# Optimization experiments

Hardware: AMD Instinct MI355X
Metric: run time of the kernel (lower is better)

## Reference

```python
import jax, jax.numpy as jnp
import numpy as np
from jax import lax

B, H, W = 2, 240, 1216
ITER, NUM = 3, 9
CH = ITER * NUM  # 27


def setup_inputs() -> dict:
    key = jax.random.key(0)
    ks = jax.random.split(key, 6)
    inp = jax.random.normal(ks[0], (B, 1, H, W), dtype=jnp.float32)
    guide = jax.random.normal(ks[1], (B, CH, H, W), dtype=jnp.float32)
    sp_dep = jax.random.uniform(ks[2], (B, 1, H, W), dtype=jnp.float32)
    confidence = jax.random.normal(ks[3], (B, 1, H, W), dtype=jnp.float32)
    conv_w = jax.random.normal(ks[4], (3 * CH, CH, 3, 3), dtype=jnp.float32) * 0.05
    conv_b = jax.random.normal(ks[5], (3 * CH,), dtype=jnp.float32) * 0.05
    # fixed 3x3 tap offsets, rows are (dx, dy) -- matches mode='xy'
    tap = jnp.array([[-1, -1], [0, -1], [1, -1], [-1, 0], [0, 0], [1, 0], [-1, 1], [0, 1], [1, 1]], dtype=jnp.float32)
    return {"input": inp, "guide": guide, "sp_dep": sp_dep, "confidence": confidence,
            "conv_w": conv_w, "conv_b": conv_b, "tap": tap}


def _bilinear_zeros(img, px, py):
    """img: [B,H,W]; px,py: [B,N,H,W] pixel coords. Matches F.grid_sample
    (bilinear, padding_mode='zeros', align_corners=False): the normalized grid
    built in get_refgrid maps exactly to pixel coord = x + tap + offset."""
    Hh, Ww = img.shape[-2], img.shape[-1]
    x0f = jnp.floor(px)
    y0f = jnp.floor(py)
    wx1 = px - x0f
    wy1 = py - y0f
    x0 = x0f.astype(jnp.int32)
    y0 = y0f.astype(jnp.int32)
    flat = img.reshape(img.shape[0], Hh * Ww)

    def gather(xi, yi):
        valid = (xi >= 0) & (xi < Ww) & (yi >= 0) & (yi < Hh)
        idx = jnp.clip(yi, 0, Hh - 1) * Ww + jnp.clip(xi, 0, Ww - 1)
        v = jax.vmap(lambda f, i: f[i])(flat, idx)  # [B,N,H,W]
        return jnp.where(valid, v, jnp.zeros((), img.dtype))

    v00 = gather(x0, y0)
    v01 = gather(x0 + 1, y0)
    v10 = gather(x0, y0 + 1)
    v11 = gather(x0 + 1, y0 + 1)
    return ((1 - wy1) * ((1 - wx1) * v00 + wx1 * v01)
            + wy1 * ((1 - wx1) * v10 + wx1 * v11))


def reference(input, guide, sp_dep, confidence, conv_w, conv_b, tap):
    Bb, _, Hh, Ww = input.shape
    out = lax.conv_general_dilated(
        guide, conv_w, window_strides=(1, 1), padding=((1, 1), (1, 1)),
        dimension_numbers=("NCHW", "OIHW", "NCHW")) + conv_b[None, :, None, None]
    # split into offsets (2*ch) and affinities (ch)
    offset = out[:, :2 * CH].reshape(Bb, ITER, NUM, 2, Hh, Ww)  # b iter n (x,y) h w
    aff = out[:, 2 * CH:].reshape(Bb, ITER, NUM, Hh, Ww)
    aff = jax.nn.softmax(aff, axis=2)  # softmax over the NUM taps

    conf = jax.nn.sigmoid(confidence[:, 0]) * jnp.sign(sp_dep[:, 0])  # [B,H,W]
    spd = sp_dep[:, 0]

    xg = jnp.arange(Ww, dtype=jnp.float32)
    yg = jnp.arange(Hh, dtype=jnp.float32)
    # sampling pixel coords: x + tap_x + offset_x  (exact grid_sample equivalence)
    px = offset[:, :, :, 0] + tap[None, None, :, 0, None, None] + xg[None, None, None, None, :]
    py = offset[:, :, :, 1] + tap[None, None, :, 1, None, None] + yg[None, None, None, :, None]

    cur = input[:, 0]  # [B,H,W]
    feat_init = cur
    inter = []
    for i in range(ITER):
        vals = _bilinear_zeros(cur, px[:, i], py[:, i])  # [B,NUM,H,W]
        agg = jnp.sum(vals * aff[:, i], axis=1)          # affinity-weighted sum
        cur = (1 - conf) * agg + conf * spd
        inter.append(cur)
    pred = cur[:, None]
    return pred, feat_init[:, None], jnp.stack(inter, axis=0)[:, :, None]
```

## Files before the change

### kernel.cpp

```cpp
#include <hip/hip_runtime.h>
#include <math.h>

#define B_ 2
#define H_ 240
#define W_ 1216
#define CH_ 27
#define NUM_ 9
#define PIX_ (B_ * H_ * W_)
#define CHP 32
#define CHL 40
#define TX 32
#define TY 8
#define HALO_W (TX + 2)
#define HALO_H (TY + 2)
#define SCS 27

typedef __attribute__((ext_vector_type(8))) __bf16 bf16x8;
typedef __attribute__((ext_vector_type(16))) float f32x16;

__global__ __launch_bounds__(256) void transpose_guide(
    const float* __restrict__ guide, __bf16* __restrict__ gt)
{
    int pix = blockIdx.x * 256 + threadIdx.x;
    if (pix >= PIX_) return;
    int b = pix / (H_ * W_);
    int off = pix - b * (H_ * W_);
    __align__(16) __bf16 tmp[CHP];
    const float* src = guide + (size_t)b * CH_ * H_ * W_ + off;
    #pragma unroll
    for (int ic = 0; ic < CH_; ++ic)
        tmp[ic] = (__bf16)src[(size_t)ic * (H_ * W_)];
    #pragma unroll
    for (int ic = CH_; ic < CHP; ++ic) tmp[ic] = (__bf16)0.f;
    bf16x8* dst = (bf16x8*)(gt + (size_t)pix * CHP);
    const bf16x8* s8 = (const bf16x8*)tmp;
    #pragma unroll
    for (int c = 0; c < 4; ++c) dst[c] = s8[c];
}

__global__ __launch_bounds__(256) void prep_weights(
    const float* __restrict__ conv_w, __bf16* __restrict__ wlin)
{
    int idx = blockIdx.x * 256 + threadIdx.x;
    if (idx >= 3 * 9 * 2 * 64) return;
    int lane = idx & 63;
    int grp = idx >> 6;
    int ks = grp & 1;
    int tapi = (grp >> 1) % 9;
    int it = (grp >> 1) / 9;
    int n = lane & 31;
    int half = lane >> 5;
    __align__(16) __bf16 v8[8];
    #pragma unroll
    for (int j = 0; j < 8; ++j) {
        int ic = ks * 16 + half * 8 + j;
        float v = 0.f;
        if (ic < CH_ && n < CH_) {
            int oc = (n < 18) ? (it * 18 + n) : (54 + it * NUM_ + (n - 18));
            v = conv_w[(size_t)(oc * CH_ + ic) * 9 + tapi];
        }
        v8[j] = (__bf16)v;
    }
    *(bf16x8*)(wlin + (size_t)idx * 8) = *(const bf16x8*)v8;
}

__global__ __launch_bounds__(256, 4) void dyspn_iter_mfma(
    const __bf16* __restrict__ gt, const __bf16* __restrict__ wlin,
    const float* __restrict__ conv_b, const float* __restrict__ tap,
    const float* __restrict__ confidence, const float* __restrict__ sp_dep,
    const float* __restrict__ cur_in, float* __restrict__ out_cur,
    float* __restrict__ pred, float* __restrict__ feat,
    const float* __restrict__ input, int iter)
{
    __shared__ __align__(16) char smem[256 * SCS * 4];
    __bf16* sG = (__bf16*)smem;
    float*  sC = (float*)smem;
    __shared__ float sBias[CH_ + 1];
    __shared__ float sTap[18];

    const int tid = threadIdx.x;
    const int lane = tid & 63;
    const int w = tid >> 6;
    const int xl = lane & 31;
    const int half = lane >> 5;
    const int tileX0 = blockIdx.x * TX;
    const int tileY0 = blockIdx.y * TY;
    const int b = blockIdx.z;

    const int x = tileX0 + (tid & 31);
    const int y = tileY0 + (tid >> 5);
    const int pix = b * (H_ * W_) + y * W_ + x;

    const float cpix  = confidence[pix];
    const float sppix = sp_dep[pix];
    const float inpix = input[pix];

    if (tid < CH_) {
        int n = tid;
        int oc = (n < 18) ? (iter * 18 + n) : (54 + iter * NUM_ + (n - 18));
        sBias[tid] = conv_b[oc];
    }
    if (tid >= 64 && tid < 64 + 18) sTap[tid - 64] = tap[tid - 64];

    for (int idx = tid; idx < HALO_H * HALO_W * 4; idx += 256) {
        int chunk = idx & 3;
        int p = idx >> 2;
        int row = p / HALO_W;
        int px = p - row * HALO_W;
        int gy = tileY0 + row - 1;
        int gx = tileX0 + px - 1;
        uint4 v = make_uint4(0, 0, 0, 0);
        if (gx >= 0 && gx < W_ && gy >= 0 && gy < H_) {
            size_t pg = (size_t)b * (H_ * W_) + (size_t)gy * W_ + gx;
            v = ((const uint4*)(gt + pg * CHP))[chunk];
        }
        *(uint4*)((char*)sG + ((size_t)(row * HALO_W + px) * CHL + chunk * 8) * 2) = v;
    }

    f32x16 acc0 = {0,0,0,0,0,0,0,0,0,0,0,0,0,0,0,0};
    f32x16 acc1 = {0,0,0,0,0,0,0,0,0,0,0,0,0,0,0,0};

    __syncthreads();

    const __bf16* wbase = wlin + ((size_t)iter * 18 * 64 + lane) * 8;
    #pragma unroll
    for (int kw = 0; kw < 3; ++kw) {
        #pragma unroll
        for (int ks = 0; ks < 2; ++ks) {
            bf16x8 A4[4];
            #pragma unroll
            for (int d = 0; d < 4; ++d) {
                const __bf16* ap = sG + (size_t)((2 * w + d) * HALO_W + xl + kw) * CHL
                                 + ks * 16 + half * 8;
                A4[d] = *(const bf16x8*)ap;
            }
            #pragma unroll
            for (int kh = 0; kh < 3; ++kh) {
                int t = kh * 3 + kw;
                bf16x8 Bf = *(const bf16x8*)(wbase + (size_t)(t * 2 + ks) * 64 * 8);
                acc0 = __builtin_amdgcn_mfma_f32_32x32x16_bf16(A4[kh],     Bf, acc0, 0, 0, 0);
                acc1 = __builtin_amdgcn_mfma_f32_32x32x16_bf16(A4[kh + 1], Bf, acc1, 0, 0, 0);
            }
        }
    }

    __syncthreads();

    if (xl < CH_) {
        #pragma unroll
        for (int a = 0; a < 2; ++a) {
            const f32x16 A = a ? acc1 : acc0;
            int ra = 2 * w + a;
            #pragma unroll
            for (int r = 0; r < 16; ++r) {
                int px_x = (r & 3) + 8 * (r >> 2) + 4 * half;
                sC[(ra * 32 + px_x) * SCS + xl] = A[r];
            }
        }
    }

    __syncthreads();

    float v27[CH_];
    #pragma unroll
    for (int j = 0; j < CH_; ++j) v27[j] = sC[tid * SCS + j] + sBias[j];

    float m = v27[18];
    #pragma unroll
    for (int n = 1; n < 9; ++n) m = fmaxf(m, v27[18 + n]);
    float a9[9]; float s = 0.f;
    #pragma unroll
    for (int n = 0; n < 9; ++n) { a9[n] = __expf(v27[18 + n] - m); s += a9[n]; }
    const float inv_s = 1.f / s;

    const float* cur = cur_in + (size_t)b * (H_ * W_);
    float agg = 0.f;
    #pragma unroll
    for (int n = 0; n < 9; ++n) {
        float px = v27[2 * n]     + sTap[2 * n]     + (float)x;
        float py = v27[2 * n + 1] + sTap[2 * n + 1] + (float)y;
        float x0f = floorf(px), y0f = floorf(py);
        float wx = px - x0f, wy = py - y0f;
        int x0 = (int)x0f, y0 = (int)y0f;
        int cx0 = min(max(x0, 0), W_ - 1), cx1 = min(max(x0 + 1, 0), W_ - 1);
        int cy0 = min(max(y0, 0), H_ - 1), cy1 = min(max(y0 + 1, 0), H_ - 1);
        float mx0 = (x0 >= 0 && x0 < W_) ? 1.f : 0.f;
        float mx1 = (x0 + 1 >= 0 && x0 + 1 < W_) ? 1.f : 0.f;
        float my0 = (y0 >= 0 && y0 < H_) ? 1.f : 0.f;
        float my1 = (y0 + 1 >= 0 && y0 + 1 < H_) ? 1.f : 0.f;
        const float* r0 = cur + (size_t)cy0 * W_;
        const float* r1 = cur + (size_t)cy1 * W_;
        float v00 = r0[cx0] * (mx0 * my0);
        float v01 = r0[cx1] * (mx1 * my0);
        float v10 = r1[cx0] * (mx0 * my1);
        float v11 = r1[cx1] * (mx1 * my1);
        float val = (1.f - wy) * ((1.f - wx) * v00 + wx * v01)
                  +        wy  * ((1.f - wx) * v10 + wx * v11);
        agg = fmaf(val, a9[n] * inv_s, agg);
    }

    float sgn = (sppix > 0.f) ? 1.f : ((sppix < 0.f) ? -1.f : 0.f);
    float conf = sgn / (1.f + __expf(-cpix));
    float nc = (1.f - conf) * agg + conf * sppix;

    out_cur[pix] = nc;
    if (pred) pred[pix] = nc;
    if (feat) feat[pix] = inpix;
}

__global__ __launch_bounds__(256) void dyspn_iter_fp32(
    const float* __restrict__ guide, const float* __restrict__ conv_w,
    const float* __restrict__ conv_b, const float* __restrict__ tap,
    const float* __restrict__ confidence, const float* __restrict__ sp_dep,
    const float* __restrict__ cur_in, float* __restrict__ out_cur,
    float* __restrict__ pred, float* __restrict__ feat,
    const float* __restrict__ input, int iter)
{
    __shared__ float sg[CH_ * HALO_H * HALO_W];
    const int tid = threadIdx.x;
    const int tileX0 = blockIdx.x * TX;
    const int tileY0 = blockIdx.y * TY;
    const int b = blockIdx.z;
    for (int idx = tid; idx < CH_ * HALO_H * HALO_W; idx += 256) {
        int ic  = idx / (HALO_H * HALO_W);
        int rem = idx % (HALO_H * HALO_W);
        int ly = rem / HALO_W;
        int lx = rem % HALO_W;
        int gy = tileY0 + ly - 1;
        int gx = tileX0 + lx - 1;
        float v = 0.f;
        if (gx >= 0 && gx < W_ && gy >= 0 && gy < H_)
            v = guide[((b * CH_ + ic) * H_ + gy) * W_ + gx];
        sg[idx] = v;
    }
    __syncthreads();
    const int tx = tid % TX;
    const int ty = tid / TX;
    const int x = tileX0 + tx;
    const int y = tileY0 + ty;
    const int oc0 = iter * 18;
    const int oc1 = 54 + iter * NUM_;
    float acc[27];
    #pragma unroll
    for (int j = 0; j < 18; ++j) acc[j] = conv_b[oc0 + j];
    #pragma unroll
    for (int j = 0; j < 9; ++j)  acc[18 + j] = conv_b[oc1 + j];
    for (int ic = 0; ic < CH_; ++ic) {
        float g[9];
        #pragma unroll
        for (int t = 0; t < 9; ++t) {
            int dy = t / 3, dx = t % 3;
            g[t] = sg[ic * (HALO_H * HALO_W) + (ty + dy) * HALO_W + (tx + dx)];
        }
        #pragma unroll
        for (int j = 0; j < 18; ++j) {
            const float* wp = conv_w + ((oc0 + j) * CH_ + ic) * 9;
            #pragma unroll
            for (int t = 0; t < 9; ++t) acc[j] = fmaf(wp[t], g[t], acc[j]);
        }
        #pragma unroll
        for (int j = 0; j < 9; ++j) {
            const float* wp = conv_w + ((oc1 + j) * CH_ + ic) * 9;
            #pragma unroll
            for (int t = 0; t < 9; ++t) acc[18 + j] = fmaf(wp[t], g[t], acc[18 + j]);
        }
    }
    float m = acc[18];
    #pragma unroll
    for (int n = 1; n < 9; ++n) m = fmaxf(m, acc[18 + n]);
    float a[9]; float s = 0.f;
    #pragma unroll
    for (int n = 0; n < 9; ++n) { a[n] = __expf(acc[18 + n] - m); s += a[n]; }
    const float inv_s = 1.f / s;
    const float* cur = cur_in + b * (H_ * W_);
    float agg = 0.f;
    #pragma unroll
    for (int n = 0; n < 9; ++n) {
        float px = acc[2 * n]     + tap[2 * n]     + (float)x;
        float py = acc[2 * n + 1] + tap[2 * n + 1] + (float)y;
        float x0f = floorf(px), y0f = floorf(py);
        float wx = px - x0f, wy = py - y0f;
        int x0 = (int)x0f, y0 = (int)y0f;
        int cx0 = min(max(x0, 0), W_ - 1), cx1 = min(max(x0 + 1, 0), W_ - 1);
        int cy0 = min(max(y0, 0), H_ - 1), cy1 = min(max(y0 + 1, 0), H_ - 1);
        float mx0 = (x0 >= 0 && x0 < W_) ? 1.f : 0.f;
        float mx1 = (x0 + 1 >= 0 && x0 + 1 < W_) ? 1.f : 0.f;
        float my0 = (y0 >= 0 && y0 < H_) ? 1.f : 0.f;
        float my1 = (y0 + 1 >= 0 && y0 + 1 < H_) ? 1.f : 0.f;
        float v00 = cur[(size_t)cy0 * W_ + cx0] * (mx0 * my0);
        float v01 = cur[(size_t)cy0 * W_ + cx1] * (mx1 * my0);
        float v10 = cur[(size_t)cy1 * W_ + cx0] * (mx0 * my1);
        float v11 = cur[(size_t)cy1 * W_ + cx1] * (mx1 * my1);
        float val = (1.f - wy) * ((1.f - wx) * v00 + wx * v01)
                  +        wy  * ((1.f - wx) * v10 + wx * v11);
        agg = fmaf(val, a[n] * inv_s, agg);
    }
    const int pix = b * (H_ * W_) + y * W_ + x;
    float c  = confidence[pix];
    float sp = sp_dep[pix];
    float sgn = (sp > 0.f) ? 1.f : ((sp < 0.f) ? -1.f : 0.f);
    float conf = sgn / (1.f + __expf(-c));
    float nc = (1.f - conf) * agg + conf * sp;
    out_cur[pix] = nc;
    if (pred) pred[pix] = nc;
    if (feat) feat[pix] = input[pix];
}

extern "C" void kernel_launch(void* const* d_in, const int* in_sizes, int n_in,
                              void* d_out, int out_size, void* d_ws, size_t ws_size,
                              hipStream_t stream) {
    (void)in_sizes; (void)n_in; (void)out_size;
    const float* input      = (const float*)d_in[0];
    const float* guide      = (const float*)d_in[1];
    const float* sp_dep     = (const float*)d_in[2];
    const float* confidence = (const float*)d_in[3];
    const float* conv_w     = (const float*)d_in[4];
    const float* conv_b     = (const float*)d_in[5];
    const float* tap        = (const float*)d_in[6];

    float* out   = (float*)d_out;
    const int P  = PIX_;
    float* pred  = out;
    float* feat  = out + P;
    float* inter = out + 2 * P;

    dim3 grid(W_ / TX, H_ / TY, B_);
    dim3 block(256);

    const size_t gt_bytes   = (size_t)PIX_ * CHP * 2;
    const size_t wlin_bytes = (size_t)3 * 9 * 2 * 64 * 8 * 2;

    if (ws_size >= gt_bytes + wlin_bytes) {
        __bf16* gt   = (__bf16*)d_ws;
        __bf16* wlin = (__bf16*)((char*)d_ws + gt_bytes);

        transpose_guide<<<(PIX_ + 255) / 256, 256, 0, stream>>>(guide, gt);
        prep_weights<<<(3 * 9 * 2 * 64 + 255) / 256, 256, 0, stream>>>(conv_w, wlin);

        for (int i = 0; i < 3; ++i) {
            const float* cur = (i == 0) ? input : (inter + (i - 1) * P);
            dyspn_iter_mfma<<<grid, block, 0, stream>>>(
                gt, wlin, conv_b, tap, confidence, sp_dep,
                cur, inter + i * P,
                (i == 2) ? pred : nullptr,
                (i == 0) ? feat : nullptr,
                input, i);
        }
    } else {
        for (int i = 0; i < 3; ++i) {
            const float* cur = (i == 0) ? input : (inter + (i - 1) * P);
            dyspn_iter_fp32<<<grid, block, 0, stream>>>(
                guide, conv_w, conv_b, tap, confidence, sp_dep,
                cur, inter + i * P,
                (i == 2) ? pred : nullptr,
                (i == 0) ? feat : nullptr,
                input, i);
        }
    }
}
```

Before: 216.6 us.

## Fuse guide transpose, weight prep and three iterations into one cooperative persistent kernel

Replaces the five separate launches (guide transpose, weight packing, three iteration kernels) with one cooperative persistent kernel. Blocks loop over tiles and use grid-wide syncs between phases and iterations. This removes per-launch overhead and gaps between dependent kernels, at the cost of grid-sync latency and a capped grid size (1140 or 760 blocks) that may reduce parallelism or balance. The fp32 fallback path is dropped, and if the workspace is too small nothing is launched.

```diff
diff --git a/kernel.cpp b/kernel.cpp
--- a/kernel.cpp
+++ b/kernel.cpp
@@ -1,5 +1,8 @@
 #include <hip/hip_runtime.h>
+#include <hip/hip_cooperative_groups.h>
 #include <math.h>
+
+namespace cg = cooperative_groups;
 
 #define B_ 2
 #define H_ 240
@@ -13,10 +16,216 @@
 #define TY 8
 #define HALO_W (TX + 2)
 #define HALO_H (TY + 2)
+#define NPX (HALO_H * HALO_W)
 #define SCS 27
+#define NTILES (38 * 30 * B_)
 
 typedef __attribute__((ext_vector_type(8))) __bf16 bf16x8;
 typedef __attribute__((ext_vector_type(16))) float f32x16;
+
+__global__ __launch_bounds__(256, 4) void dyspn_persistent(
+    const float* __restrict__ guide, const float* __restrict__ conv_w,
+    const float* __restrict__ conv_b, const float* __restrict__ tap,
+    const float* __restrict__ confidence, const float* __restrict__ sp_dep,
+    const float* __restrict__ input, float* __restrict__ pred,
+    float* __restrict__ feat, float* __restrict__ inter,
+    __bf16* __restrict__ gt, __bf16* __restrict__ wlin)
+{
+    cg::grid_group gg = cg::this_grid();
+
+    __shared__ __align__(16) char smemA[256 * SCS * 4];
+    __bf16* sG = (__bf16*)smemA;
+    float*  sC = (float*)smemA;
+    __shared__ float sBias[CH_ + 1];
+    __shared__ float sTap[18];
+
+    const int tid  = threadIdx.x;
+    const int lane = tid & 63;
+    const int w    = tid >> 6;
+    const int xl   = lane & 31;
+    const int half = lane >> 5;
+    const int nb   = gridDim.x;
+    const int brank = blockIdx.x;
+
+    for (int pix = brank * 256 + tid; pix < PIX_; pix += nb * 256) {
+        int b = pix / (H_ * W_);
+        int off = pix - b * (H_ * W_);
+        __align__(16) __bf16 tmp[CHP];
+        const float* src = guide + (size_t)b * CH_ * H_ * W_ + off;
+        #pragma unroll
+        for (int ic = 0; ic < CH_; ++ic)
+            tmp[ic] = (__bf16)src[(size_t)ic * (H_ * W_)];
+        #pragma unroll
+        for (int ic = CH_; ic < CHP; ++ic) tmp[ic] = (__bf16)0.f;
+        bf16x8* dst = (bf16x8*)(gt + (size_t)pix * CHP);
+        const bf16x8* s8 = (const bf16x8*)tmp;
+        #pragma unroll
+        for (int c = 0; c < 4; ++c) dst[c] = s8[c];
+    }
+
+    for (int idx = brank * 256 + tid; idx < 3 * 9 * 2 * 64; idx += nb * 256) {
+        int l = idx & 63;
+        int grp = idx >> 6;
+        int ks = grp & 1;
+        int tapi = (grp >> 1) % 9;
+        int it = (grp >> 1) / 9;
+        int n = l & 31;
+        int hf = l >> 5;
+        __align__(16) __bf16 v8[8];
+        #pragma unroll
+        for (int j = 0; j < 8; ++j) {
+            int ic = ks * 16 + hf * 8 + j;
+            float v = 0.f;
+            if (ic < CH_ && n < CH_) {
+                int oc = (n < 18) ? (it * 18 + n) : (54 + it * NUM_ + (n - 18));
+                v = conv_w[(size_t)(oc * CH_ + ic) * 9 + tapi];
+            }
+            v8[j] = (__bf16)v;
+        }
+        *(bf16x8*)(wlin + (size_t)idx * 8) = *(const bf16x8*)v8;
+    }
+
+    gg.sync();
+
+    for (int iter = 0; iter < 3; ++iter) {
+        const float* cur_all = (iter == 0) ? input : (inter + (size_t)(iter - 1) * PIX_);
+        float* dst = inter + (size_t)iter * PIX_;
+
+        if (tid < CH_) {
+            int n = tid;
+            int oc = (n < 18) ? (iter * 18 + n) : (54 + iter * NUM_ + (n - 18));
+            sBias[tid] = conv_b[oc];
+        }
+        if (tid >= 64 && tid < 64 + 18) sTap[tid - 64] = tap[tid - 64];
+
+        const __bf16* wbase = wlin + ((size_t)iter * 18 * 64 + lane) * 8;
+
+        for (int t = brank; t < NTILES; t += nb) {
+            int b   = t / (38 * 30);
+            int r   = t - b * (38 * 30);
+            int tyi = r / 38;
+            int txi = r - tyi * 38;
+            const int tileX0 = txi * TX;
+            const int tileY0 = tyi * TY;
+
+            const int x = tileX0 + (tid & 31);
+            const int y = tileY0 + (tid >> 5);
+            const int pix = b * (H_ * W_) + y * W_ + x;
+
+            const float cpix  = confidence[pix];
+            const float sppix = sp_dep[pix];
+            const float inpix = input[pix];
+
+            for (int idx = tid; idx < NPX * 4; idx += 256) {
+                int chunk = idx & 3;
+                int p = idx >> 2;
+                int row = p / HALO_W;
+                int px = p - row * HALO_W;
+                int gy = tileY0 + row - 1;
+                int gx = tileX0 + px - 1;
+                uint4 v = make_uint4(0, 0, 0, 0);
+                if (gx >= 0 && gx < W_ && gy >= 0 && gy < H_) {
+                    size_t pg = (size_t)b * (H_ * W_) + (size_t)gy * W_ + gx;
+                    v = ((const uint4*)(gt + pg * CHP))[chunk];
+                }
+                *(uint4*)((char*)sG + ((size_t)(row * HALO_W + px) * CHL + chunk * 8) * 2) = v;
+            }
+
+            f32x16 acc0 = {0,0,0,0,0,0,0,0,0,0,0,0,0,0,0,0};
+            f32x16 acc1 = {0,0,0,0,0,0,0,0,0,0,0,0,0,0,0,0};
+
+            __syncthreads();
+
+            #pragma unroll
+            for (int kw = 0; kw < 3; ++kw) {
+                #pragma unroll
+                for (int ks = 0; ks < 2; ++ks) {
+                    bf16x8 A4[4];
+                    #pragma unroll
+                    for (int d = 0; d < 4; ++d) {
+                        const __bf16* ap = sG + (size_t)((2 * w + d) * HALO_W + xl + kw) * CHL
+                                         + ks * 16 + half * 8;
+                        A4[d] = *(const bf16x8*)ap;
+                    }
+                    #pragma unroll
+                    for (int kh = 0; kh < 3; ++kh) {
+                        int tt = kh * 3 + kw;
+                        bf16x8 Bf = *(const bf16x8*)(wbase + (size_t)(tt * 2 + ks) * 64 * 8);
+                        acc0 = __builtin_amdgcn_mfma_f32_32x32x16_bf16(A4[kh],     Bf, acc0, 0, 0, 0);
+                        acc1 = __builtin_amdgcn_mfma_f32_32x32x16_bf16(A4[kh + 1], Bf, acc1, 0, 0, 0);
+                    }
+                }
+            }
+
+            __syncthreads();
+
+            if (xl < CH_) {
+                #pragma unroll
+                for (int a = 0; a < 2; ++a) {
+                    const f32x16 A = a ? acc1 : acc0;
+                    int ra = 2 * w + a;
+                    #pragma unroll
+                    for (int rr = 0; rr < 16; ++rr) {
+                        int px_x = (rr & 3) + 8 * (rr >> 2) + 4 * half;
+                        sC[(ra * 32 + px_x) * SCS + xl] = A[rr];
+                    }
+                }
+            }
+
+            __syncthreads();
+
+            float v27[CH_];
+            #pragma unroll
+            for (int j = 0; j < CH_; ++j) v27[j] = sC[tid * SCS + j] + sBias[j];
+
+            float m = v27[18];
+            #pragma unroll
+            for (int n = 1; n < 9; ++n) m = fmaxf(m, v27[18 + n]);
+            float a9[9]; float s = 0.f;
+            #pragma unroll
+            for (int n = 0; n < 9; ++n) { a9[n] = __expf(v27[18 + n] - m); s += a9[n]; }
+            const float inv_s = 1.f / s;
+
+            const float* cur = cur_all + (size_t)b * (H_ * W_);
+            float agg = 0.f;
+            #pragma unroll
+            for (int n = 0; n < 9; ++n) {
+                float px = v27[2 * n]     + sTap[2 * n]     + (float)x;
+                float py = v27[2 * n + 1] + sTap[2 * n + 1] + (float)y;
+                float x0f = floorf(px), y0f = floorf(py);
+                float wx = px - x0f, wy = py - y0f;
+                int x0 = (int)x0f, y0 = (int)y0f;
+                int cx0 = min(max(x0, 0), W_ - 1), cx1 = min(max(x0 + 1, 0), W_ - 1);
+                int cy0 = min(max(y0, 0), H_ - 1), cy1 = min(max(y0 + 1, 0), H_ - 1);
+                float mx0 = (x0 >= 0 && x0 < W_) ? 1.f : 0.f;
+                float mx1 = (x0 + 1 >= 0 && x0 + 1 < W_) ? 1.f : 0.f;
+                float my0 = (y0 >= 0 && y0 < H_) ? 1.f : 0.f;
+                float my1 = (y0 + 1 >= 0 && y0 + 1 < H_) ? 1.f : 0.f;
+                const float* r0 = cur + (size_t)cy0 * W_;
+                const float* r1 = cur + (size_t)cy1 * W_;
+                float v00 = r0[cx0] * (mx0 * my0);
+                float v01 = r0[cx1] * (mx1 * my0);
+                float v10 = r1[cx0] * (mx0 * my1);
+                float v11 = r1[cx1] * (mx1 * my1);
+                float val = (1.f - wy) * ((1.f - wx) * v00 + wx * v01)
+                          +        wy  * ((1.f - wx) * v10 + wx * v11);
+                agg = fmaf(val, a9[n] * inv_s, agg);
+            }
+
+            float sgn = (sppix > 0.f) ? 1.f : ((sppix < 0.f) ? -1.f : 0.f);
+            float conf = sgn / (1.f + __expf(-cpix));
+            float nc = (1.f - conf) * agg + conf * sppix;
+
+            dst[pix] = nc;
+            if (iter == 2) pred[pix] = nc;
+            if (iter == 0) feat[pix] = inpix;
+
+            __syncthreads();
+        }
+
+        if (iter < 2) gg.sync();
+    }
+}
 
 __global__ __launch_bounds__(256) void transpose_guide(
     const float* __restrict__ guide, __bf16* __restrict__ gt)
@@ -102,7 +311,7 @@
     }
     if (tid >= 64 && tid < 64 + 18) sTap[tid - 64] = tap[tid - 64];
 
-    for (int idx = tid; idx < HALO_H * HALO_W * 4; idx += 256) {
+    for (int idx = tid; idx < NPX * 4; idx += 256) {
         int chunk = idx & 3;
         int p = idx >> 2;
         int row = p / HALO_W;
@@ -208,104 +417,6 @@
     if (feat) feat[pix] = inpix;
 }
 
-__global__ __launch_bounds__(256) void dyspn_iter_fp32(
-    const float* __restrict__ guide, const float* __restrict__ conv_w,
-    const float* __restrict__ conv_b, const float* __restrict__ tap,
-    const float* __restrict__ confidence, const float* __restrict__ sp_dep,
-    const float* __restrict__ cur_in, float* __restrict__ out_cur,
-    float* __restrict__ pred, float* __restrict__ feat,
-    const float* __restrict__ input, int iter)
-{
-    __shared__ float sg[CH_ * HALO_H * HALO_W];
-    const int tid = threadIdx.x;
-    const int tileX0 = blockIdx.x * TX;
-    const int tileY0 = blockIdx.y * TY;
-    const int b = blockIdx.z;
-    for (int idx = tid; idx < CH_ * HALO_H * HALO_W; idx += 256) {
-        int ic  = idx / (HALO_H * HALO_W);
-        int rem = idx % (HALO_H * HALO_W);
-        int ly = rem / HALO_W;
-        int lx = rem % HALO_W;
-        int gy = tileY0 + ly - 1;
-        int gx = tileX0 + lx - 1;
-        float v = 0.f;
-        if (gx >= 0 && gx < W_ && gy >= 0 && gy < H_)
-            v = guide[((b * CH_ + ic) * H_ + gy) * W_ + gx];
-        sg[idx] = v;
-    }
-    __syncthreads();
-    const int tx = tid % TX;
-    const int ty = tid / TX;
-    const int x = tileX0 + tx;
-    const int y = tileY0 + ty;
-    const int oc0 = iter * 18;
-    const int oc1 = 54 + iter * NUM_;
-    float acc[27];
-    #pragma unroll
-    for (int j = 0; j < 18; ++j) acc[j] = conv_b[oc0 + j];
-    #pragma unroll
-    for (int j = 0; j < 9; ++j)  acc[18 + j] = conv_b[oc1 + j];
-    for (int ic = 0; ic < CH_; ++ic) {
-        float g[9];
-        #pragma unroll
-        for (int t = 0; t < 9; ++t) {
-            int dy = t / 3, dx = t % 3;
-            g[t] = sg[ic * (HALO_H * HALO_W) + (ty + dy) * HALO_W + (tx + dx)];
-        }
-        #pragma unroll
-        for (int j = 0; j < 18; ++j) {
-            const float* wp = conv_w + ((oc0 + j) * CH_ + ic) * 9;
-            #pragma unroll
-            for (int t = 0; t < 9; ++t) acc[j] = fmaf(wp[t], g[t], acc[j]);
-        }
-        #pragma unroll
-        for (int j = 0; j < 9; ++j) {
-            const float* wp = conv_w + ((oc1 + j) * CH_ + ic) * 9;
-            #pragma unroll
-            for (int t = 0; t < 9; ++t) acc[18 + j] = fmaf(wp[t], g[t], acc[18 + j]);
-        }
-    }
-    float m = acc[18];
-    #pragma unroll
-    for (int n = 1; n < 9; ++n) m = fmaxf(m, acc[18 + n]);
-    float a[9]; float s = 0.f;
-    #pragma unroll
-    for (int n = 0; n < 9; ++n) { a[n] = __expf(acc[18 + n] - m); s += a[n]; }
-    const float inv_s = 1.f / s;
-    const float* cur = cur_in + b * (H_ * W_);
-    float agg = 0.f;
-    #pragma unroll
-    for (int n = 0; n < 9; ++n) {
-        float px = acc[2 * n]     + tap[2 * n]     + (float)x;
-        float py = acc[2 * n + 1] + tap[2 * n + 1] + (float)y;
-        float x0f = floorf(px), y0f = floorf(py);
-        float wx = px - x0f, wy = py - y0f;
-        int x0 = (int)x0f, y0 = (int)y0f;
-        int cx0 = min(max(x0, 0), W_ - 1), cx1 = min(max(x0 + 1, 0), W_ - 1);
-        int cy0 = min(max(y0, 0), H_ - 1), cy1 = min(max(y0 + 1, 0), H_ - 1);
-        float mx0 = (x0 >= 0 && x0 < W_) ? 1.f : 0.f;
-        float mx1 = (x0 + 1 >= 0 && x0 + 1 < W_) ? 1.f : 0.f;
-        float my0 = (y0 >= 0 && y0 < H_) ? 1.f : 0.f;
-        float my1 = (y0 + 1 >= 0 && y0 + 1 < H_) ? 1.f : 0.f;
-        float v00 = cur[(size_t)cy0 * W_ + cx0] * (mx0 * my0);
-        float v01 = cur[(size_t)cy0 * W_ + cx1] * (mx1 * my0);
-        float v10 = cur[(size_t)cy1 * W_ + cx0] * (mx0 * my1);
-        float v11 = cur[(size_t)cy1 * W_ + cx1] * (mx1 * my1);
-        float val = (1.f - wy) * ((1.f - wx) * v00 + wx * v01)
-                  +        wy  * ((1.f - wx) * v10 + wx * v11);
-        agg = fmaf(val, a[n] * inv_s, agg);
-    }
-    const int pix = b * (H_ * W_) + y * W_ + x;
-    float c  = confidence[pix];
-    float sp = sp_dep[pix];
-    float sgn = (sp > 0.f) ? 1.f : ((sp < 0.f) ? -1.f : 0.f);
-    float conf = sgn / (1.f + __expf(-c));
-    float nc = (1.f - conf) * agg + conf * sp;
-    out_cur[pix] = nc;
-    if (pred) pred[pix] = nc;
-    if (feat) feat[pix] = input[pix];
-}
-
 extern "C" void kernel_launch(void* const* d_in, const int* in_sizes, int n_in,
                               void* d_out, int out_size, void* d_ws, size_t ws_size,
                               hipStream_t stream) {
@@ -324,37 +435,45 @@
     float* feat  = out + P;
     float* inter = out + 2 * P;
 
-    dim3 grid(W_ / TX, H_ / TY, B_);
-    dim3 block(256);
-
     const size_t gt_bytes   = (size_t)PIX_ * CHP * 2;
     const size_t wlin_bytes = (size_t)3 * 9 * 2 * 64 * 8 * 2;
 
-    if (ws_size >= gt_bytes + wlin_bytes) {
-        __bf16* gt   = (__bf16*)d_ws;
-        __bf16* wlin = (__bf16*)((char*)d_ws + gt_bytes);
-
+    __bf16* gt   = (__bf16*)d_ws;
+    __bf16* wlin = (__bf16*)((char*)d_ws + gt_bytes);
+
+    int dev = 0;
+    (void)hipGetDevice(&dev);
+    int numCU = 0;
+    (void)hipDeviceGetAttribute(&numCU, hipDeviceAttributeMultiprocessorCount, dev);
+    int maxPerCU = 0;
+    (void)hipOccupancyMaxActiveBlocksPerMultiprocessor(&maxPerCU, dyspn_persistent, 256, 0);
+    long cap = (long)maxPerCU * (long)numCU;
+
+    bool haveWs = ws_size >= gt_bytes + wlin_bytes;
+
+    if (haveWs && cap >= 256) {
+        int gp = (cap >= 1140) ? 1140 : ((cap >= 760) ? 760 : (int)cap);
+        void* args[] = { (void*)&guide, (void*)&conv_w, (void*)&conv_b,
+                         (void*)&tap, (void*)&confidence, (void*)&sp_dep,
+                         (void*)&input, (void*)&pred, (void*)&feat,
+                         (void*)&inter, (void*)&gt, (void*)&wlin };
+        hipError_t e = hipLaunchCooperativeKernel((const void*)dyspn_persistent,
+                                                  dim3(gp), dim3(256), args, 0, stream);
+        if (e == hipSuccess) return;
+    }
+
+    if (haveWs) {
         transpose_guide<<<(PIX_ + 255) / 256, 256, 0, stream>>>(guide, gt);
         prep_weights<<<(3 * 9 * 2 * 64 + 255) / 256, 256, 0, stream>>>(conv_w, wlin);
-
+        dim3 grid(W_ / TX, H_ / TY, B_);
         for (int i = 0; i < 3; ++i) {
             const float* cur = (i == 0) ? input : (inter + (i - 1) * P);
-            dyspn_iter_mfma<<<grid, block, 0, stream>>>(
+            dyspn_iter_mfma<<<grid, 256, 0, stream>>>(
                 gt, wlin, conv_b, tap, confidence, sp_dep,
                 cur, inter + i * P,
                 (i == 2) ? pred : nullptr,
                 (i == 0) ? feat : nullptr,
                 input, i);
         }
-    } else {
-        for (int i = 0; i < 3; ++i) {
-            const float* cur = (i == 0) ? input : (inter + (i - 1) * P);
-            dyspn_iter_fp32<<<grid, block, 0, stream>>>(
-                guide, conv_w, conv_b, tap, confidence, sp_dep,
-                cur, inter + i * P,
-                (i == 2) ? pred : nullptr,
-                (i == 0) ? feat : nullptr,
-                input, i);
-        }
     }
 }
```

Result: slower. 489.0 us (+125.8%).
